# Kernel optimization log

Hardware: AMD Instinct MI355X
Metric: run time of the kernel (lower is better)

## Reference

```python
import jax, jax.numpy as jnp
import numpy as np

B, S, D = 2, 1024, 2048
H, G, DK, DV = 16, 4, 128, 128
E, K, F = 8, 2, 4096
EPS = 1e-6


def _rms_norm(x, w):
    return x * jax.lax.rsqrt(jnp.mean(x * x, axis=-1, keepdims=True) + EPS) * w


def _rope(x):
    # x: [B, S, h, d]; rotate-half RoPE with base 10000
    d = x.shape[-1]
    half = d // 2
    inv_freq = 1.0 / (10000.0 ** (jnp.arange(half, dtype=jnp.float32) / half))
    ang = jnp.arange(x.shape[1], dtype=jnp.float32)[:, None] * inv_freq[None, :]  # [S, half]
    cos = jnp.cos(ang)[None, :, None, :]
    sin = jnp.sin(ang)[None, :, None, :]
    x1, x2 = x[..., :half], x[..., half:]
    return jnp.concatenate([x1 * cos - x2 * sin, x1 * sin + x2 * cos], axis=-1)


def setup_inputs() -> dict:
    key = jax.random.key(0)
    ks = jax.random.split(key, 10)
    s = lambda *shape: 1.0 / np.sqrt(shape[-2] if len(shape) > 1 else shape[0])
    inp = {
        "x": jax.random.normal(ks[0], (B, S, D), jnp.float32),
        "ln1_w": jnp.ones((D,), jnp.float32),
        "Wq": jax.random.normal(ks[1], (D, H * DK), jnp.float32) * (D ** -0.5),
        "Wk": jax.random.normal(ks[2], (D, G * DK), jnp.float32) * (D ** -0.5),
        "Wv": jax.random.normal(ks[3], (D, G * DV), jnp.float32) * (D ** -0.5),
        "Wo": jax.random.normal(ks[4], (H * DV, D), jnp.float32) * ((H * DV) ** -0.5),
        "ln2_w": jnp.ones((D,), jnp.float32),
        "Wr": jax.random.normal(ks[5], (D, E), jnp.float32) * (D ** -0.5),
        "W1": jax.random.normal(ks[6], (E, D, F), jnp.float32) * (D ** -0.5),
        "W2": jax.random.normal(ks[7], (E, F, D), jnp.float32) * (F ** -0.5),
    }
    return inp


def reference(x, ln1_w, Wq, Wk, Wv, Wo, ln2_w, Wr, W1, W2):
    # --- GQA attention (pre-norm, residual) ---
    h = _rms_norm(x, ln1_w)
    q = (h @ Wq).reshape(B, S, H, DK)
    k = (h @ Wk).reshape(B, S, G, DK)
    v = (h @ Wv).reshape(B, S, G, DV)
    q = _rope(q)
    k = _rope(k)
    # expand KV groups to all heads: each group serves H // G query heads
    rep = H // G
    k = jnp.repeat(k, rep, axis=2)  # [B, S, H, DK]
    v = jnp.repeat(v, rep, axis=2)  # [B, S, H, DV]
    scores = jnp.einsum("bshd,bthd->bhst", q, k) * (DK ** -0.5)  # [B,H,S,S]
    causal = jnp.tril(jnp.ones((S, S), bool))
    scores = jnp.where(causal[None, None], scores, jnp.finfo(scores.dtype).min)
    probs = jax.nn.softmax(scores, axis=-1)
    attn = jnp.einsum("bhst,bthd->bshd", probs, v).reshape(B, S, H * DV)
    x = x + attn @ Wo

    # --- top-k MoE MLP (pre-norm, residual) ---
    h = _rms_norm(x, ln2_w)
    t = h.reshape(B * S, D)  # tokens
    logits = t @ Wr  # [T, E]
    top_vals, top_idx = jax.lax.top_k(logits, K)
    gates = jax.nn.softmax(top_vals, axis=-1)  # [T, K]
    # dense combine weights [T, E] (zero for non-selected experts)
    comb = jnp.zeros((B * S, E), t.dtype)
    comb = comb.at[jnp.arange(B * S)[:, None], top_idx].set(gates)
    # dense all-expert compute (reference form of the grouped GEMM)
    mid = jax.nn.silu(jnp.einsum("td,edf->tef", t, W1))  # [T, E, F]
    out_e = jnp.einsum("tef,efd->ted", mid, W2)          # [T, E, D]
    moe = jnp.einsum("te,ted->td", comb, out_e).reshape(B, S, D)
    return x + moe
```

## Files before the change

### kernel.cpp

```cpp
#include <hip/hip_runtime.h>

typedef unsigned short u16;
typedef __attribute__((ext_vector_type(8))) short bf16x8;
typedef __attribute__((ext_vector_type(4))) float f32x4;

__device__ __forceinline__ u16 f2bf(float f) {
  union { float f; unsigned u; } v; v.f = f;
  unsigned r = (v.u + 0x7fffu + ((v.u >> 16) & 1u)) >> 16;
  return (u16)r;
}
__device__ __forceinline__ float bf2f(u16 u) {
  union { unsigned u; float f; } v; v.u = ((unsigned)u) << 16;
  return v.f;
}
__device__ __forceinline__ void split2(float f, u16& hi, u16& lo) {
  hi = f2bf(f);
  lo = f2bf(f - bf2f(hi));
}

typedef const unsigned int __attribute__((address_space(1)))* gptr_t;
typedef unsigned int __attribute__((address_space(3)))* lptr_t;

__device__ __forceinline__ void gl16(const u16* g, u16* l) {
#if __has_builtin(__builtin_amdgcn_global_load_lds)
  __builtin_amdgcn_global_load_lds((gptr_t)g, (lptr_t)l, 16, 0, 0);
#else
  *reinterpret_cast<uint4*>(l) = *reinterpret_cast<const uint4*>(g);
#endif
}


__device__ __forceinline__ void mf_bf16(const u16* __restrict__ sA,
    const u16* __restrict__ sB, f32x4 (&acc)[4][4], int wm, int wn, int lr, int lk) {
  bf16x8 a[4], b[4];
#pragma unroll
  for (int i = 0; i < 4; i++) {
    a[i] = *reinterpret_cast<const bf16x8*>(&sA[(wm + i * 16 + lr) * 32 + lk]);
    b[i] = *reinterpret_cast<const bf16x8*>(&sB[(wn + i * 16 + lr) * 32 + lk]);
  }
#pragma unroll
  for (int i = 0; i < 4; i++)
#pragma unroll
    for (int j = 0; j < 4; j++)
      acc[i][j] = __builtin_amdgcn_mfma_f32_16x16x32_bf16(a[i], b[j], acc[i][j], 0, 0, 0);
}

__device__ __forceinline__ void mf_hilo(const u16* __restrict__ sAhp,
    const u16* __restrict__ sAlp, const u16* __restrict__ sBhp,
    const u16* __restrict__ sBlp, f32x4 (&acc)[4][4], int wm, int wn, int lr, int lk) {
  bf16x8 ah[4], al[4], bh[4], bl[4];
#pragma unroll
  for (int i = 0; i < 4; i++) {
    ah[i] = *reinterpret_cast<const bf16x8*>(&sAhp[(wm + i * 16 + lr) * 32 + lk]);
    al[i] = *reinterpret_cast<const bf16x8*>(&sAlp[(wm + i * 16 + lr) * 32 + lk]);
    bh[i] = *reinterpret_cast<const bf16x8*>(&sBhp[(wn + i * 16 + lr) * 32 + lk]);
    bl[i] = *reinterpret_cast<const bf16x8*>(&sBlp[(wn + i * 16 + lr) * 32 + lk]);
  }
#pragma unroll
  for (int i = 0; i < 4; i++)
#pragma unroll
    for (int j = 0; j < 4; j++) {
      f32x4 t = acc[i][j];
      t = __builtin_amdgcn_mfma_f32_16x16x32_bf16(al[i], bh[j], t, 0, 0, 0);
      t = __builtin_amdgcn_mfma_f32_16x16x32_bf16(ah[i], bl[j], t, 0, 0, 0);
      t = __builtin_amdgcn_mfma_f32_16x16x32_bf16(ah[i], bh[j], t, 0, 0, 0);
      acc[i][j] = t;
    }
}

#define HILO_PREAMBLE \
  __shared__ __align__(16) u16 sAh[2][4096], sAl[2][4096], sBh[2][4096], sBl[2][4096]; \
  int tid = threadIdx.x, lane = tid & 63; \
  int wm = ((tid >> 6) & 1) << 6, wn = (tid >> 7) << 6; \
  int lr = lane & 15, lk = (lane >> 4) << 3; \
  int er = (lane >> 4) << 2, ec = lane & 15; \
  int r = tid >> 2, c = (tid & 3) << 3; \
  int so = r * 32 + c, so2 = so + 2048; \
  f32x4 acc[4][4] = {};

#define STAGE_HILO(buf) \
  gl16(pAh + ko, &sAh[buf][so]); gl16(pAh2 + ko, &sAh[buf][so2]); \
  gl16(pAl + ko, &sAl[buf][so]); gl16(pAl2 + ko, &sAl[buf][so2]); \
  gl16(pBh + ko, &sBh[buf][so]); gl16(pBh2 + ko, &sBh[buf][so2]); \
  gl16(pBl + ko, &sBl[buf][so]); gl16(pBl2 + ko, &sBl[buf][so2]);

#define BF16_PREAMBLE \
  __shared__ __align__(16) u16 sA[2][4096], sB[2][4096]; \
  int tid = threadIdx.x, lane = tid & 63; \
  int wm = ((tid >> 6) & 1) << 6, wn = (tid >> 7) << 6; \
  int lr = lane & 15, lk = (lane >> 4) << 3; \
  int er = (lane >> 4) << 2, ec = lane & 15; \
  int r = tid >> 2, c = (tid & 3) << 3; \
  int so = r * 32 + c, so2 = so + 2048; \
  f32x4 acc[4][4] = {};

#define STAGE_AB(buf) \
  gl16(pA + ko, &sA[buf][so]); gl16(pA2 + ko, &sA[buf][so2]); \
  gl16(pB + ko, &sB[buf][so]); gl16(pB2 + ko, &sB[buf][so2]);

__global__ __launch_bounds__(256) void convt_bf16(const float* __restrict__ W,
    u16* __restrict__ T, int K, int N) {
  __shared__ float t[64][33];
  long eo = (long)blockIdx.z * K * N;
  int k0 = blockIdx.y << 6, n0 = blockIdx.x << 5;
  int tid = threadIdx.x;
  int r = tid >> 3, cc = (tid & 7) << 2;
  const float* src = W + eo + (long)(k0 + r) * N + n0 + cc;
  float4 a = *reinterpret_cast<const float4*>(src);
  float4 b = *reinterpret_cast<const float4*>(src + (long)32 * N);
  t[r][cc] = a.x; t[r][cc + 1] = a.y; t[r][cc + 2] = a.z; t[r][cc + 3] = a.w;
  t[r + 32][cc] = b.x; t[r + 32][cc + 1] = b.y; t[r + 32][cc + 2] = b.z; t[r + 32][cc + 3] = b.w;
  __syncthreads();
  int n = tid >> 3, kc = (tid & 7) << 3;
  __align__(16) u16 h[8];
#pragma unroll
  for (int i = 0; i < 8; i++) h[i] = f2bf(t[kc + i][n]);
  *reinterpret_cast<uint4*>(&T[eo + (long)(n0 + n) * K + k0 + kc]) =
      *reinterpret_cast<uint4*>(h);
}

__global__ __launch_bounds__(256) void convt_split(const float* __restrict__ W,
    u16* __restrict__ Thi, u16* __restrict__ Tlo, int K, int N) {
  __shared__ float t[64][33];
  int k0 = blockIdx.y << 6, n0 = blockIdx.x << 5;
  int tid = threadIdx.x;
  int r = tid >> 3, cc = (tid & 7) << 2;
  const float* src = W + (long)(k0 + r) * N + n0 + cc;
  float4 a = *reinterpret_cast<const float4*>(src);
  float4 b = *reinterpret_cast<const float4*>(src + (long)32 * N);
  t[r][cc] = a.x; t[r][cc + 1] = a.y; t[r][cc + 2] = a.z; t[r][cc + 3] = a.w;
  t[r + 32][cc] = b.x; t[r + 32][cc + 1] = b.y; t[r + 32][cc + 2] = b.z; t[r + 32][cc + 3] = b.w;
  __syncthreads();
  int n = tid >> 3, kc = (tid & 7) << 3;
  __align__(16) u16 h[8], l[8];
#pragma unroll
  for (int i = 0; i < 8; i++) split2(t[kc + i][n], h[i], l[i]);
  long o = (long)(n0 + n) * K + k0 + kc;
  *reinterpret_cast<uint4*>(&Thi[o]) = *reinterpret_cast<uint4*>(h);
  *reinterpret_cast<uint4*>(&Tlo[o]) = *reinterpret_cast<uint4*>(l);
}


__global__ __launch_bounds__(256) void rmsnorm_split(const float* __restrict__ x,
    const float* __restrict__ w, u16* __restrict__ ohi, u16* __restrict__ olo) {
  __shared__ float lbuf[4];
  int tid = threadIdx.x;
  long base = (long)blockIdx.x * 2048;
  float4 v0 = *reinterpret_cast<const float4*>(&x[base + tid * 8]);
  float4 v1 = *reinterpret_cast<const float4*>(&x[base + tid * 8 + 4]);
  float ss = v0.x * v0.x + v0.y * v0.y + v0.z * v0.z + v0.w * v0.w +
             v1.x * v1.x + v1.y * v1.y + v1.z * v1.z + v1.w * v1.w;
  for (int off = 32; off; off >>= 1) ss += __shfl_down(ss, off);
  if ((tid & 63) == 0) lbuf[tid >> 6] = ss;
  __syncthreads();
  float tot = lbuf[0] + lbuf[1] + lbuf[2] + lbuf[3];
  float scale = 1.0f / sqrtf(tot * (1.0f / 2048.0f) + 1e-6f);
  float4 w0 = *reinterpret_cast<const float4*>(&w[tid * 8]);
  float4 w1 = *reinterpret_cast<const float4*>(&w[tid * 8 + 4]);
  float f[8] = {v0.x * scale * w0.x, v0.y * scale * w0.y, v0.z * scale * w0.z,
                v0.w * scale * w0.w, v1.x * scale * w1.x, v1.y * scale * w1.y,
                v1.z * scale * w1.z, v1.w * scale * w1.w};
  __align__(16) u16 h[8], l[8];
#pragma unroll
  for (int i = 0; i < 8; i++) split2(f[i], h[i], l[i]);
  *reinterpret_cast<uint4*>(&ohi[base + tid * 8]) = *reinterpret_cast<uint4*>(h);
  *reinterpret_cast<uint4*>(&olo[base + tid * 8]) = *reinterpret_cast<uint4*>(l);
}

__global__ __launch_bounds__(256) void rmsnorm_bf16(const float* __restrict__ x,
    const float* __restrict__ w, u16* __restrict__ o) {
  __shared__ float lbuf[4];
  int tid = threadIdx.x;
  long base = (long)blockIdx.x * 2048;
  float4 v0 = *reinterpret_cast<const float4*>(&x[base + tid * 8]);
  float4 v1 = *reinterpret_cast<const float4*>(&x[base + tid * 8 + 4]);
  float ss = v0.x * v0.x + v0.y * v0.y + v0.z * v0.z + v0.w * v0.w +
             v1.x * v1.x + v1.y * v1.y + v1.z * v1.z + v1.w * v1.w;
  for (int off = 32; off; off >>= 1) ss += __shfl_down(ss, off);
  if ((tid & 63) == 0) lbuf[tid >> 6] = ss;
  __syncthreads();
  float tot = lbuf[0] + lbuf[1] + lbuf[2] + lbuf[3];
  float scale = 1.0f / sqrtf(tot * (1.0f / 2048.0f) + 1e-6f);
  float4 w0 = *reinterpret_cast<const float4*>(&w[tid * 8]);
  float4 w1 = *reinterpret_cast<const float4*>(&w[tid * 8 + 4]);
  ushort4 o0, o1;
  o0.x = f2bf(v0.x * scale * w0.x); o0.y = f2bf(v0.y * scale * w0.y);
  o0.z = f2bf(v0.z * scale * w0.z); o0.w = f2bf(v0.w * scale * w0.w);
  o1.x = f2bf(v1.x * scale * w1.x); o1.y = f2bf(v1.y * scale * w1.y);
  o1.z = f2bf(v1.z * scale * w1.z); o1.w = f2bf(v1.w * scale * w1.w);
  *reinterpret_cast<ushort4*>(&o[base + tid * 8]) = o0;
  *reinterpret_cast<ushort4*>(&o[base + tid * 8 + 4]) = o1;
}

__global__ __launch_bounds__(256) void rope_split(const float* __restrict__ x, int nh,
    u16* __restrict__ ohi, u16* __restrict__ olo) {
  int unit = blockIdx.x * 4 + (threadIdx.x >> 6);
  int lane = threadIdx.x & 63;
  int s = (unit / nh) & 1023;
  const float* p = x + (long)unit * 128;
  float x1 = p[lane], x2 = p[lane + 64];
  float ang = (float)s * exp2f((float)lane * (-13.287712379549449f / 64.0f));
  float sn, cs;
  sincosf(ang, &sn, &cs);
  long o = (long)unit * 128 + lane;
  u16 hh, ll;
  split2(x1 * cs - x2 * sn, hh, ll);
  ohi[o] = hh; olo[o] = ll;
  split2(x1 * sn + x2 * cs, hh, ll);
  ohi[o + 64] = hh; olo[o + 64] = ll;
}

__global__ __launch_bounds__(256) void transpose_split(const float* __restrict__ in,
    u16* __restrict__ ohi, u16* __restrict__ olo, int R, int C) {
  __shared__ float tile[32][33];
  long bo = (long)blockIdx.z * R * C;
  int r0 = blockIdx.y * 32, c0 = blockIdx.x * 32;
  int r = threadIdx.x >> 5, c = threadIdx.x & 31;
#pragma unroll
  for (int i = 0; i < 4; i++)
    tile[r + i * 8][c] = in[bo + (long)(r0 + r + i * 8) * C + c0 + c];
  __syncthreads();
#pragma unroll
  for (int i = 0; i < 4; i++) {
    u16 hh, ll;
    split2(tile[c][r + i * 8], hh, ll);
    long o = bo + (long)(c0 + r + i * 8) * R + r0 + c;
    ohi[o] = hh; olo[o] = ll;
  }
}

__global__ __launch_bounds__(256) void softmax_split(const float* __restrict__ sc,
    u16* __restrict__ phi, u16* __restrict__ plo) {
  __shared__ float lbuf[4];
  long row = blockIdx.x;
  int q = (int)(row & 1023);
  const float* p = sc + row * 1024;
  int tid = threadIdx.x;
  int valid = q + 1;
  int pend = (q & ~127) + 128;
  float v[4];
  float mx = -1e30f;
#pragma unroll
  for (int i = 0; i < 4; i++) {
    int t = tid + i * 256;
    float f = (t < valid) ? p[t] : -1e30f;
    v[i] = f;
    mx = fmaxf(mx, f);
  }
  for (int off = 32; off; off >>= 1) mx = fmaxf(mx, __shfl_down(mx, off));
  if ((tid & 63) == 0) lbuf[tid >> 6] = mx;
  __syncthreads();
  float m = fmaxf(fmaxf(lbuf[0], lbuf[1]), fmaxf(lbuf[2], lbuf[3]));
  __syncthreads();
  float sum = 0.0f;
#pragma unroll
  for (int i = 0; i < 4; i++) {
    int t = tid + i * 256;
    float e = (t < valid) ? expf(v[i] - m) : 0.0f;
    v[i] = e;
    sum += e;
  }
  for (int off = 32; off; off >>= 1) sum += __shfl_down(sum, off);
  if ((tid & 63) == 0) lbuf[tid >> 6] = sum;
  __syncthreads();
  float inv = 1.0f / (lbuf[0] + lbuf[1] + lbuf[2] + lbuf[3]);
#pragma unroll
  for (int i = 0; i < 4; i++) {
    int t = tid + i * 256;
    if (t < valid) {
      u16 hh, ll;
      split2(v[i] * inv, hh, ll);
      phi[row * 1024 + t] = hh; plo[row * 1024 + t] = ll;
    } else if (t < pend) {
      phi[row * 1024 + t] = 0; plo[row * 1024 + t] = 0;
    }
  }
}

__global__ __launch_bounds__(256) void router_kernel(const float* __restrict__ xo,
    const float* __restrict__ w, const float* __restrict__ Wr,
    int* __restrict__ tok_e, float* __restrict__ tok_g, int* __restrict__ counts) {
  __shared__ float lbuf[32];
  int tid = threadIdx.x;
  long base = (long)blockIdx.x * 2048;
  float4 v0 = *reinterpret_cast<const float4*>(&xo[base + tid * 8]);
  float4 v1 = *reinterpret_cast<const float4*>(&xo[base + tid * 8 + 4]);
  float ss = v0.x * v0.x + v0.y * v0.y + v0.z * v0.z + v0.w * v0.w +
             v1.x * v1.x + v1.y * v1.y + v1.z * v1.z + v1.w * v1.w;
  for (int off = 32; off; off >>= 1) ss += __shfl_down(ss, off);
  if ((tid & 63) == 0) lbuf[tid >> 6] = ss;
  __syncthreads();
  float tot = lbuf[0] + lbuf[1] + lbuf[2] + lbuf[3];
  float scale = 1.0f / sqrtf(tot * (1.0f / 2048.0f) + 1e-6f);
  __syncthreads();
  float4 w0 = *reinterpret_cast<const float4*>(&w[tid * 8]);
  float4 w1 = *reinterpret_cast<const float4*>(&w[tid * 8 + 4]);
  float h[8] = {v0.x * scale * w0.x, v0.y * scale * w0.y, v0.z * scale * w0.z,
                v0.w * scale * w0.w, v1.x * scale * w1.x, v1.y * scale * w1.y,
                v1.z * scale * w1.z, v1.w * scale * w1.w};
  float part[8] = {0, 0, 0, 0, 0, 0, 0, 0};
#pragma unroll
  for (int j = 0; j < 8; j++) {
    const float* wr = Wr + (long)(tid * 8 + j) * 8;
    float4 a = *reinterpret_cast<const float4*>(wr);
    float4 b = *reinterpret_cast<const float4*>(wr + 4);
    part[0] += h[j] * a.x; part[1] += h[j] * a.y;
    part[2] += h[j] * a.z; part[3] += h[j] * a.w;
    part[4] += h[j] * b.x; part[5] += h[j] * b.y;
    part[6] += h[j] * b.z; part[7] += h[j] * b.w;
  }
#pragma unroll
  for (int e = 0; e < 8; e++) {
    float s = part[e];
    for (int off = 32; off; off >>= 1) s += __shfl_down(s, off);
    if ((tid & 63) == 0) lbuf[(tid >> 6) * 8 + e] = s;
  }
  __syncthreads();
  if (tid == 0) {
    float lg[8];
#pragma unroll
    for (int e = 0; e < 8; e++)
      lg[e] = lbuf[e] + lbuf[8 + e] + lbuf[16 + e] + lbuf[24 + e];
    int e1 = 0;
    for (int e = 1; e < 8; e++) if (lg[e] > lg[e1]) e1 = e;
    int e2 = -1;
    for (int e = 0; e < 8; e++) if (e != e1 && (e2 < 0 || lg[e] > lg[e2])) e2 = e;
    float ex = __expf(lg[e2] - lg[e1]);
    float g1 = 1.0f / (1.0f + ex);
    tok_e[blockIdx.x * 2] = e1; tok_e[blockIdx.x * 2 + 1] = e2;
    tok_g[blockIdx.x * 2] = g1; tok_g[blockIdx.x * 2 + 1] = 1.0f - g1;
    atomicAdd(&counts[e1], 1);
    atomicAdd(&counts[e2], 1);
  }
}

__global__ void scan8(const int* __restrict__ counts, int* __restrict__ offsets,
                      int* __restrict__ cursor) {
  if (threadIdx.x == 0) {
    int off = 0;
    for (int e = 0; e < 8; e++) { offsets[e] = off; off += counts[e]; cursor[e] = 0; }
  }
}

__global__ __launch_bounds__(256) void fill_lists(const int* __restrict__ tok_e,
    const float* __restrict__ tok_g, const int* __restrict__ offsets,
    int* __restrict__ cursor, int* __restrict__ ltok, float* __restrict__ lgate) {
  int idx = blockIdx.x * 256 + threadIdx.x;
  int token = idx >> 1;
  int e = tok_e[idx];
  float g = tok_g[idx];
  int pos = atomicAdd(&cursor[e], 1);
  int j = offsets[e] + pos;
  ltok[j] = token;
  lgate[j] = g;
}


__global__ __launch_bounds__(256) void gemm_hilo(
    const u16* __restrict__ Ahi, const u16* __restrict__ Alo, long ldA,
    const u16* __restrict__ Bhi, const u16* __restrict__ Blo, long ldB,
    const float* __restrict__ resid, float* __restrict__ C, long ldC, int Ksize) {
  HILO_PREAMBLE
  int m0 = blockIdx.y << 7, n0 = blockIdx.x << 7;
  const u16* pAh = Ahi + (long)(m0 + r) * ldA + c;  const u16* pAh2 = pAh + 64 * ldA;
  const u16* pAl = Alo + (long)(m0 + r) * ldA + c;  const u16* pAl2 = pAl + 64 * ldA;
  const u16* pBh = Bhi + (long)(n0 + r) * ldB + c;  const u16* pBh2 = pBh + 64 * ldB;
  const u16* pBl = Blo + (long)(n0 + r) * ldB + c;  const u16* pBl2 = pBl + 64 * ldB;
  { int ko = 0; STAGE_HILO(0) }
  __syncthreads();
  int cur = 0;
  for (int k0 = 0; k0 < Ksize; k0 += 32) {
    if (k0 + 32 < Ksize) { int ko = k0 + 32; STAGE_HILO(cur ^ 1) }
    mf_hilo(sAh[cur], sAl[cur], sBh[cur], sBl[cur], acc, wm, wn, lr, lk);
    __syncthreads();
    cur ^= 1;
  }
#pragma unroll
  for (int i = 0; i < 4; i++)
#pragma unroll
    for (int j = 0; j < 4; j++)
#pragma unroll
      for (int rr = 0; rr < 4; rr++) {
        long idx = (long)(m0 + wm + i * 16 + er + rr) * ldC + n0 + wn + j * 16 + ec;
        float v = acc[i][j][rr];
        C[idx] = resid ? resid[idx] + v : v;
      }
}

__global__ __launch_bounds__(256) void gemm_qk(
    const u16* __restrict__ qhi, const u16* __restrict__ qlo,
    const u16* __restrict__ khi, const u16* __restrict__ klo,
    float* __restrict__ sc, int bh0) {
  HILO_PREAMBLE
  int idx = blockIdx.x, mi = 0;
  while ((mi + 1) * (mi + 2) / 2 <= idx) mi++;
  int ni = idx - mi * (mi + 1) / 2;
  int bh = bh0 + blockIdx.y, b = bh >> 4, hd = bh & 15, g = hd >> 2;
  int m0 = mi << 7, n0 = ni << 7;
  const u16* pAh = qhi + (long)b * 2097152 + hd * 128 + (long)(m0 + r) * 2048 + c;
  const u16* pAh2 = pAh + 64 * 2048;
  const u16* pAl = qlo + (long)b * 2097152 + hd * 128 + (long)(m0 + r) * 2048 + c;
  const u16* pAl2 = pAl + 64 * 2048;
  const u16* pBh = khi + (long)b * 524288 + g * 128 + (long)(n0 + r) * 512 + c;
  const u16* pBh2 = pBh + 64 * 512;
  const u16* pBl = klo + (long)b * 524288 + g * 128 + (long)(n0 + r) * 512 + c;
  const u16* pBl2 = pBl + 64 * 512;
  { int ko = 0; STAGE_HILO(0) }
  __syncthreads();
  int cur = 0;
  for (int k0 = 0; k0 < 128; k0 += 32) {
    if (k0 + 32 < 128) { int ko = k0 + 32; STAGE_HILO(cur ^ 1) }
    mf_hilo(sAh[cur], sAl[cur], sBh[cur], sBl[cur], acc, wm, wn, lr, lk);
    __syncthreads();
    cur ^= 1;
  }
  float* Cb = sc + ((long)blockIdx.y * 1024 + m0) * 1024 + n0;
  const float scalef = 0.08838834764831845f;
#pragma unroll
  for (int i = 0; i < 4; i++)
#pragma unroll
    for (int j = 0; j < 4; j++)
#pragma unroll
      for (int rr = 0; rr < 4; rr++)
        Cb[(long)(wm + i * 16 + er + rr) * 1024 + wn + j * 16 + ec] =
            acc[i][j][rr] * scalef;
}

__global__ __launch_bounds__(256) void gemm_pv(
    const u16* __restrict__ phi, const u16* __restrict__ plo,
    const u16* __restrict__ vthi, const u16* __restrict__ vtlo,
    u16* __restrict__ athi, u16* __restrict__ atlo, int bh0) {
  HILO_PREAMBLE
  int m0 = blockIdx.x << 7;
  int bh = bh0 + blockIdx.y, b = bh >> 4, hd = bh & 15, g = hd >> 2;
  const u16* pAh = phi + (long)blockIdx.y * 1048576 + (long)(m0 + r) * 1024 + c;
  const u16* pAh2 = pAh + 64 * 1024;
  const u16* pAl = plo + (long)blockIdx.y * 1048576 + (long)(m0 + r) * 1024 + c;
  const u16* pAl2 = pAl + 64 * 1024;
  const u16* pBh = vthi + (long)(b * 4 + g) * 131072 + (long)r * 1024 + c;
  const u16* pBh2 = pBh + 64 * 1024;
  const u16* pBl = vtlo + (long)(b * 4 + g) * 131072 + (long)r * 1024 + c;
  const u16* pBl2 = pBl + 64 * 1024;
  int Klim = m0 + 128;
  { int ko = 0; STAGE_HILO(0) }
  __syncthreads();
  int cur = 0;
  for (int k0 = 0; k0 < Klim; k0 += 32) {
    if (k0 + 32 < Klim) { int ko = k0 + 32; STAGE_HILO(cur ^ 1) }
    mf_hilo(sAh[cur], sAl[cur], sBh[cur], sBl[cur], acc, wm, wn, lr, lk);
    __syncthreads();
    cur ^= 1;
  }
  long Cb = ((long)(b * 1024 + m0) * 16 + hd) * 128;
#pragma unroll
  for (int i = 0; i < 4; i++)
#pragma unroll
    for (int j = 0; j < 4; j++)
#pragma unroll
      for (int rr = 0; rr < 4; rr++) {
        u16 hh, ll;
        split2(acc[i][j][rr], hh, ll);
        long o = Cb + (long)(wm + i * 16 + er + rr) * 2048 + wn + j * 16 + ec;
        athi[o] = hh; atlo[o] = ll;
      }
}


__global__ __launch_bounds__(256) void gemm_moe1(const u16* __restrict__ t2,
    const u16* __restrict__ W1T, const int* __restrict__ offsets,
    const int* __restrict__ counts, const int* __restrict__ ltok,
    u16* __restrict__ mid) {
  int e = blockIdx.z;
  int cnt = counts[e];
  int m0 = blockIdx.y << 7;
  if (m0 >= cnt) return;
  BF16_PREAMBLE
  int off = offsets[e];
  int n0 = blockIdx.x << 7;
  int valid = cnt - m0; if (valid > 128) valid = 128;
  int rr0 = (r < valid) ? r : 0;
  int rr1 = (r + 64 < valid) ? (r + 64) : 0;
  const u16* pA = t2 + (long)ltok[off + m0 + rr0] * 2048 + c;
  const u16* pA2 = t2 + (long)ltok[off + m0 + rr1] * 2048 + c;
  const u16* pB = W1T + (long)e * 8388608 + (long)(n0 + r) * 2048 + c;
  const u16* pB2 = pB + 64 * 2048;
  { int ko = 0; STAGE_AB(0) }
  __syncthreads();
  int cur = 0;
  for (int k0 = 0; k0 < 2048; k0 += 32) {
    if (k0 + 32 < 2048) { int ko = k0 + 32; STAGE_AB(cur ^ 1) }
    mf_bf16(sA[cur], sB[cur], acc, wm, wn, lr, lk);
    __syncthreads();
    cur ^= 1;
  }
#pragma unroll
  for (int i = 0; i < 4; i++)
#pragma unroll
    for (int j = 0; j < 4; j++)
#pragma unroll
      for (int rr = 0; rr < 4; rr++) {
        int rowl = wm + i * 16 + er + rr;
        if (rowl < valid) {
          float v = acc[i][j][rr];
          v = v / (1.0f + __expf(-v));
          mid[(long)(off + m0 + rowl) * 4096 + n0 + wn + j * 16 + ec] = f2bf(v);
        }
      }
}

__global__ __launch_bounds__(256) void gemm_moe2(const u16* __restrict__ mid,
    const u16* __restrict__ W2T, const int* __restrict__ offsets,
    const int* __restrict__ counts, const int* __restrict__ ltok,
    const float* __restrict__ lgate, float* __restrict__ out) {
  int e = blockIdx.z;
  int cnt = counts[e];
  int m0 = blockIdx.y << 7;
  if (m0 >= cnt) return;
  BF16_PREAMBLE
  int off = offsets[e];
  int n0 = blockIdx.x << 7;
  int valid = cnt - m0; if (valid > 128) valid = 128;
  int rw0 = off + m0 + ((r < valid) ? r : valid - 1);
  int rw1 = off + m0 + ((r + 64 < valid) ? r + 64 : valid - 1);
  const u16* pA = mid + (long)rw0 * 4096 + c;
  const u16* pA2 = mid + (long)rw1 * 4096 + c;
  const u16* pB = W2T + (long)e * 8388608 + (long)(n0 + r) * 4096 + c;
  const u16* pB2 = pB + 64 * 4096;
  { int ko = 0; STAGE_AB(0) }
  __syncthreads();
  int cur = 0;
  for (int k0 = 0; k0 < 4096; k0 += 32) {
    if (k0 + 32 < 4096) { int ko = k0 + 32; STAGE_AB(cur ^ 1) }
    mf_bf16(sA[cur], sB[cur], acc, wm, wn, lr, lk);
    __syncthreads();
    cur ^= 1;
  }
#pragma unroll
  for (int i = 0; i < 4; i++)
#pragma unroll
    for (int j = 0; j < 4; j++)
#pragma unroll
      for (int rr = 0; rr < 4; rr++) {
        int rowl = wm + i * 16 + er + rr;
        if (rowl < valid) {
          int t = ltok[off + m0 + rowl];
          float g = lgate[off + m0 + rowl];
          atomicAdd(&out[(long)t * 2048 + n0 + wn + j * 16 + ec], g * acc[i][j][rr]);
        }
      }
}

extern "C" void kernel_launch(void* const* d_in, const int* in_sizes, int n_in,
                              void* d_out, int out_size, void* d_ws, size_t ws_size,
                              hipStream_t stream) {
  (void)in_sizes; (void)n_in; (void)out_size; (void)ws_size;
  const float* x   = (const float*)d_in[0];
  const float* ln1 = (const float*)d_in[1];
  const float* Wq  = (const float*)d_in[2];
  const float* Wk  = (const float*)d_in[3];
  const float* Wv  = (const float*)d_in[4];
  const float* Wo  = (const float*)d_in[5];
  const float* ln2 = (const float*)d_in[6];
  const float* Wr  = (const float*)d_in[7];
  const float* W1  = (const float*)d_in[8];
  const float* W2  = (const float*)d_in[9];
  float* out = (float*)d_out;
  char* ws = (char*)d_ws;

  float* sc  = (float*)(ws);
  u16* phi   = (u16*)(ws + 33554432);
  u16* plo   = (u16*)(ws + 50331648);
  u16* hhi   = (u16*)(ws + 67108864);
  u16* hlo   = (u16*)(ws + 75497472);
  float* q   = (float*)(ws + 83886080);
  float* kk  = (float*)(ws + 100663296);
  float* vv  = (float*)(ws + 104857600);
  u16* qhi   = (u16*)(ws + 109051904);
  u16* qlo   = (u16*)(ws + 117440512);
  u16* khi   = (u16*)(ws + 125829120);
  u16* klo   = (u16*)(ws + 127926272);
  u16* vthi  = (u16*)(ws + 130023424);
  u16* vtlo  = (u16*)(ws + 132120576);
  u16* athi  = (u16*)(ws + 134217728);
  u16* atlo  = (u16*)(ws + 142606336);
  u16* wqh   = (u16*)(ws + 150994944);
  u16* wql   = (u16*)(ws + 159383552);
  u16* wkh   = (u16*)(ws + 167772160);
  u16* wkl   = (u16*)(ws + 169869312);
  u16* wvh   = (u16*)(ws + 171966464);
  u16* wvl   = (u16*)(ws + 174063616);
  u16* woh   = (u16*)(ws + 176160768);
  u16* wol   = (u16*)(ws + 184549376);
  u16* wbuf  = (u16*)(ws);
  u16* mid   = (u16*)(ws + 134217728);
  u16* t2    = (u16*)(ws + 167772160);
  char* misc = ws + 176160768;
  int*   tok_e   = (int*)misc;
  float* tok_g   = (float*)(misc + 16384);
  int*   ltok    = (int*)(misc + 32768);
  float* lgate   = (float*)(misc + 49152);
  int*   counts  = (int*)(misc + 65536);
  int*   offsets = (int*)(misc + 65600);
  int*   cursor  = (int*)(misc + 65664);

  convt_split<<<dim3(64, 32), 256, 0, stream>>>(Wq, wqh, wql, 2048, 2048);
  convt_split<<<dim3(16, 32), 256, 0, stream>>>(Wk, wkh, wkl, 2048, 512);
  convt_split<<<dim3(16, 32), 256, 0, stream>>>(Wv, wvh, wvl, 2048, 512);
  convt_split<<<dim3(64, 32), 256, 0, stream>>>(Wo, woh, wol, 2048, 2048);

  rmsnorm_split<<<2048, 256, 0, stream>>>(x, ln1, hhi, hlo);
  gemm_hilo<<<dim3(16, 16), 256, 0, stream>>>(hhi, hlo, 2048, wqh, wql, 2048,
                                              nullptr, q, 2048, 2048);
  gemm_hilo<<<dim3(4, 16), 256, 0, stream>>>(hhi, hlo, 2048, wkh, wkl, 2048,
                                             nullptr, kk, 512, 2048);
  gemm_hilo<<<dim3(4, 16), 256, 0, stream>>>(hhi, hlo, 2048, wvh, wvl, 2048,
                                             nullptr, vv, 512, 2048);
  rope_split<<<8192, 256, 0, stream>>>(q, 16, qhi, qlo);
  rope_split<<<2048, 256, 0, stream>>>(kk, 4, khi, klo);
  transpose_split<<<dim3(16, 32, 2), 256, 0, stream>>>(vv, vthi, vtlo, 1024, 512);
  for (int s = 0; s < 4; s++) {
    gemm_qk<<<dim3(36, 8), 256, 0, stream>>>(qhi, qlo, khi, klo, sc, s * 8);
    softmax_split<<<8192, 256, 0, stream>>>(sc, phi, plo);
    gemm_pv<<<dim3(8, 8), 256, 0, stream>>>(phi, plo, vthi, vtlo, athi, atlo, s * 8);
  }
  gemm_hilo<<<dim3(16, 16), 256, 0, stream>>>(athi, atlo, 2048, woh, wol, 2048,
                                              x, out, 2048, 2048);
  rmsnorm_bf16<<<2048, 256, 0, stream>>>(out, ln2, t2);
  hipMemsetAsync(counts, 0, 32, stream);
  router_kernel<<<2048, 256, 0, stream>>>(out, ln2, Wr, tok_e, tok_g, counts);
  scan8<<<1, 64, 0, stream>>>(counts, offsets, cursor);
  fill_lists<<<16, 256, 0, stream>>>(tok_e, tok_g, offsets, cursor, ltok, lgate);
  convt_bf16<<<dim3(128, 32, 8), 256, 0, stream>>>(W1, wbuf, 2048, 4096);
  gemm_moe1<<<dim3(32, 16, 8), 256, 0, stream>>>(t2, wbuf, offsets, counts, ltok, mid);
  convt_bf16<<<dim3(64, 64, 8), 256, 0, stream>>>(W2, wbuf, 4096, 2048);
  gemm_moe2<<<dim3(16, 16, 8), 256, 0, stream>>>(mid, wbuf, offsets, counts, ltok,
                                                 lgate, out);
}
```

Before: 1.566 ms.

## Split-K GEMMs, fuse QKV projection, and process all heads in one attention pass

Concatenates Wq/Wk/Wv into one weight and runs a single QKV GEMM with split-K over two partial buffers, which the RoPE and transpose kernels then sum. Attention now runs all 32 heads in one launch: QK writes hi/lo bf16 scores directly, softmax works in place on them, and PV is split by key tile over a triangular grid with atomic accumulation into fp32. Wo and MoE2 also use split-K with atomics, raising block count to fill more CUs. The cost is extra memsets, atomic traffic and additional partial-sum reads, and the fp32 accumulation order becomes nondeterministic.

```diff
diff --git a/kernel.cpp b/kernel.cpp
--- a/kernel.cpp
+++ b/kernel.cpp
@@ -28,7 +28,6 @@
   *reinterpret_cast<uint4*>(l) = *reinterpret_cast<const uint4*>(g);
 #endif
 }
-
 
 __device__ __forceinline__ void mf_bf16(const u16* __restrict__ sA,
     const u16* __restrict__ sB, f32x4 (&acc)[4][4], int wm, int wn, int lr, int lk) {
@@ -192,33 +191,39 @@
   *reinterpret_cast<ushort4*>(&o[base + tid * 8 + 4]) = o1;
 }
 
-__global__ __launch_bounds__(256) void rope_split(const float* __restrict__ x, int nh,
+__global__ __launch_bounds__(256) void rope2_split(const float* __restrict__ x0,
+    const float* __restrict__ x1, int hshift, int hmask, long ld, long colbase,
     u16* __restrict__ ohi, u16* __restrict__ olo) {
   int unit = blockIdx.x * 4 + (threadIdx.x >> 6);
   int lane = threadIdx.x & 63;
-  int s = (unit / nh) & 1023;
-  const float* p = x + (long)unit * 128;
-  float x1 = p[lane], x2 = p[lane + 64];
+  int s = (unit >> hshift) & 1023;
+  long src = (long)(unit >> hshift) * ld + colbase + ((long)(unit & hmask) << 7);
+  float a1 = x0[src + lane] + x1[src + lane];
+  float a2 = x0[src + lane + 64] + x1[src + lane + 64];
   float ang = (float)s * exp2f((float)lane * (-13.287712379549449f / 64.0f));
   float sn, cs;
   sincosf(ang, &sn, &cs);
   long o = (long)unit * 128 + lane;
   u16 hh, ll;
-  split2(x1 * cs - x2 * sn, hh, ll);
+  split2(a1 * cs - a2 * sn, hh, ll);
   ohi[o] = hh; olo[o] = ll;
-  split2(x1 * sn + x2 * cs, hh, ll);
+  split2(a1 * sn + a2 * cs, hh, ll);
   ohi[o + 64] = hh; olo[o + 64] = ll;
 }
 
-__global__ __launch_bounds__(256) void transpose_split(const float* __restrict__ in,
-    u16* __restrict__ ohi, u16* __restrict__ olo, int R, int C) {
+__global__ __launch_bounds__(256) void transpose2_split(const float* __restrict__ in0,
+    const float* __restrict__ in1, long ld, long bstride, u16* __restrict__ ohi,
+    u16* __restrict__ olo, int R, int C) {
   __shared__ float tile[32][33];
+  long bi = (long)blockIdx.z * bstride;
   long bo = (long)blockIdx.z * R * C;
   int r0 = blockIdx.y * 32, c0 = blockIdx.x * 32;
   int r = threadIdx.x >> 5, c = threadIdx.x & 31;
 #pragma unroll
-  for (int i = 0; i < 4; i++)
-    tile[r + i * 8][c] = in[bo + (long)(r0 + r + i * 8) * C + c0 + c];
+  for (int i = 0; i < 4; i++) {
+    long a = bi + (long)(r0 + r + i * 8) * ld + c0 + c;
+    tile[r + i * 8][c] = in0[a] + in1[a];
+  }
   __syncthreads();
 #pragma unroll
   for (int i = 0; i < 4; i++) {
@@ -229,23 +234,25 @@
   }
 }
 
-__global__ __launch_bounds__(256) void softmax_split(const float* __restrict__ sc,
-    u16* __restrict__ phi, u16* __restrict__ plo) {
+__global__ __launch_bounds__(256) void softmax_hilo(u16* __restrict__ ph,
+    u16* __restrict__ pl) {
   __shared__ float lbuf[4];
   long row = blockIdx.x;
   int q = (int)(row & 1023);
-  const float* p = sc + row * 1024;
   int tid = threadIdx.x;
   int valid = q + 1;
   int pend = (q & ~127) + 128;
-  float v[4];
+  int t0 = tid * 4;
+  long base = row * 1024 + t0;
+  ushort4 vh = *reinterpret_cast<ushort4*>(&ph[base]);
+  ushort4 vl = *reinterpret_cast<ushort4*>(&pl[base]);
+  float v[4] = {bf2f(vh.x) + bf2f(vl.x), bf2f(vh.y) + bf2f(vl.y),
+                bf2f(vh.z) + bf2f(vl.z), bf2f(vh.w) + bf2f(vl.w)};
   float mx = -1e30f;
 #pragma unroll
   for (int i = 0; i < 4; i++) {
-    int t = tid + i * 256;
-    float f = (t < valid) ? p[t] : -1e30f;
-    v[i] = f;
-    mx = fmaxf(mx, f);
+    if (t0 + i >= valid) v[i] = -1e30f;
+    mx = fmaxf(mx, v[i]);
   }
   for (int off = 32; off; off >>= 1) mx = fmaxf(mx, __shfl_down(mx, off));
   if ((tid & 63) == 0) lbuf[tid >> 6] = mx;
@@ -255,8 +262,7 @@
   float sum = 0.0f;
 #pragma unroll
   for (int i = 0; i < 4; i++) {
-    int t = tid + i * 256;
-    float e = (t < valid) ? expf(v[i] - m) : 0.0f;
+    float e = (t0 + i < valid) ? expf(v[i] - m) : 0.0f;
     v[i] = e;
     sum += e;
   }
@@ -264,17 +270,29 @@
   if ((tid & 63) == 0) lbuf[tid >> 6] = sum;
   __syncthreads();
   float inv = 1.0f / (lbuf[0] + lbuf[1] + lbuf[2] + lbuf[3]);
-#pragma unroll
-  for (int i = 0; i < 4; i++) {
-    int t = tid + i * 256;
-    if (t < valid) {
-      u16 hh, ll;
-      split2(v[i] * inv, hh, ll);
-      phi[row * 1024 + t] = hh; plo[row * 1024 + t] = ll;
-    } else if (t < pend) {
-      phi[row * 1024 + t] = 0; plo[row * 1024 + t] = 0;
-    }
-  }
+  if (t0 < pend) {
+    ushort4 oh, ol;
+    u16 hh, ll;
+    split2(v[0] * inv, hh, ll); oh.x = hh; ol.x = ll;
+    split2(v[1] * inv, hh, ll); oh.y = hh; ol.y = ll;
+    split2(v[2] * inv, hh, ll); oh.z = hh; ol.z = ll;
+    split2(v[3] * inv, hh, ll); oh.w = hh; ol.w = ll;
+    *reinterpret_cast<ushort4*>(&ph[base]) = oh;
+    *reinterpret_cast<ushort4*>(&pl[base]) = ol;
+  }
+}
+
+__global__ __launch_bounds__(256) void split_attn(const float* __restrict__ a,
+    u16* __restrict__ ohi, u16* __restrict__ olo) {
+  long i = ((long)blockIdx.x * 256 + threadIdx.x) * 8;
+  float4 v0 = *reinterpret_cast<const float4*>(&a[i]);
+  float4 v1 = *reinterpret_cast<const float4*>(&a[i + 4]);
+  float f[8] = {v0.x, v0.y, v0.z, v0.w, v1.x, v1.y, v1.z, v1.w};
+  __align__(16) u16 h[8], l[8];
+#pragma unroll
+  for (int j = 0; j < 8; j++) split2(f[j], h[j], l[j]);
+  *reinterpret_cast<uint4*>(&ohi[i]) = *reinterpret_cast<uint4*>(h);
+  *reinterpret_cast<uint4*>(&olo[i]) = *reinterpret_cast<uint4*>(l);
 }
 
 __global__ __launch_bounds__(256) void router_kernel(const float* __restrict__ xo,
@@ -356,46 +374,80 @@
 }
 
 
-__global__ __launch_bounds__(256) void gemm_hilo(
-    const u16* __restrict__ Ahi, const u16* __restrict__ Alo, long ldA,
-    const u16* __restrict__ Bhi, const u16* __restrict__ Blo, long ldB,
-    const float* __restrict__ resid, float* __restrict__ C, long ldC, int Ksize) {
+__global__ __launch_bounds__(256) void gemm_qkv(
+    const u16* __restrict__ Ahi, const u16* __restrict__ Alo,
+    const u16* __restrict__ Bhi, const u16* __restrict__ Blo,
+    float* __restrict__ C0, float* __restrict__ C1) {
   HILO_PREAMBLE
   int m0 = blockIdx.y << 7, n0 = blockIdx.x << 7;
-  const u16* pAh = Ahi + (long)(m0 + r) * ldA + c;  const u16* pAh2 = pAh + 64 * ldA;
-  const u16* pAl = Alo + (long)(m0 + r) * ldA + c;  const u16* pAl2 = pAl + 64 * ldA;
-  const u16* pBh = Bhi + (long)(n0 + r) * ldB + c;  const u16* pBh2 = pBh + 64 * ldB;
-  const u16* pBl = Blo + (long)(n0 + r) * ldB + c;  const u16* pBl2 = pBl + 64 * ldB;
+  long kb = (long)blockIdx.z << 10;
+  const u16* pAh = Ahi + (long)(m0 + r) * 2048 + kb + c;  const u16* pAh2 = pAh + 64 * 2048;
+  const u16* pAl = Alo + (long)(m0 + r) * 2048 + kb + c;  const u16* pAl2 = pAl + 64 * 2048;
+  const u16* pBh = Bhi + (long)(n0 + r) * 2048 + kb + c;  const u16* pBh2 = pBh + 64 * 2048;
+  const u16* pBl = Blo + (long)(n0 + r) * 2048 + kb + c;  const u16* pBl2 = pBl + 64 * 2048;
   { int ko = 0; STAGE_HILO(0) }
   __syncthreads();
   int cur = 0;
-  for (int k0 = 0; k0 < Ksize; k0 += 32) {
-    if (k0 + 32 < Ksize) { int ko = k0 + 32; STAGE_HILO(cur ^ 1) }
+  for (int k0 = 0; k0 < 1024; k0 += 32) {
+    if (k0 + 32 < 1024) { int ko = k0 + 32; STAGE_HILO(cur ^ 1) }
     mf_hilo(sAh[cur], sAl[cur], sBh[cur], sBl[cur], acc, wm, wn, lr, lk);
     __syncthreads();
     cur ^= 1;
   }
+  float* C = blockIdx.z ? C1 : C0;
 #pragma unroll
   for (int i = 0; i < 4; i++)
 #pragma unroll
     for (int j = 0; j < 4; j++)
 #pragma unroll
+      for (int rr = 0; rr < 4; rr++)
+        C[(long)(m0 + wm + i * 16 + er + rr) * 3072 + n0 + wn + j * 16 + ec] =
+            acc[i][j][rr];
+}
+
+__global__ __launch_bounds__(256) void gemm_wo(
+    const u16* __restrict__ Ahi, const u16* __restrict__ Alo,
+    const u16* __restrict__ Bhi, const u16* __restrict__ Blo,
+    const float* __restrict__ resid, float* __restrict__ C) {
+  HILO_PREAMBLE
+  int m0 = blockIdx.y << 7, n0 = blockIdx.x << 7;
+  long kb = (long)blockIdx.z << 10;
+  const u16* pAh = Ahi + (long)(m0 + r) * 2048 + kb + c;  const u16* pAh2 = pAh + 64 * 2048;
+  const u16* pAl = Alo + (long)(m0 + r) * 2048 + kb + c;  const u16* pAl2 = pAl + 64 * 2048;
+  const u16* pBh = Bhi + (long)(n0 + r) * 2048 + kb + c;  const u16* pBh2 = pBh + 64 * 2048;
+  const u16* pBl = Blo + (long)(n0 + r) * 2048 + kb + c;  const u16* pBl2 = pBl + 64 * 2048;
+  { int ko = 0; STAGE_HILO(0) }
+  __syncthreads();
+  int cur = 0;
+  for (int k0 = 0; k0 < 1024; k0 += 32) {
+    if (k0 + 32 < 1024) { int ko = k0 + 32; STAGE_HILO(cur ^ 1) }
+    mf_hilo(sAh[cur], sAl[cur], sBh[cur], sBl[cur], acc, wm, wn, lr, lk);
+    __syncthreads();
+    cur ^= 1;
+  }
+  int addres = (blockIdx.z == 0);
+#pragma unroll
+  for (int i = 0; i < 4; i++)
+#pragma unroll
+    for (int j = 0; j < 4; j++)
+#pragma unroll
       for (int rr = 0; rr < 4; rr++) {
-        long idx = (long)(m0 + wm + i * 16 + er + rr) * ldC + n0 + wn + j * 16 + ec;
+        long idx = (long)(m0 + wm + i * 16 + er + rr) * 2048 + n0 + wn + j * 16 + ec;
         float v = acc[i][j][rr];
-        C[idx] = resid ? resid[idx] + v : v;
+        if (addres) v += resid[idx];
+        atomicAdd(&C[idx], v);
       }
 }
 
 __global__ __launch_bounds__(256) void gemm_qk(
     const u16* __restrict__ qhi, const u16* __restrict__ qlo,
     const u16* __restrict__ khi, const u16* __restrict__ klo,
-    float* __restrict__ sc, int bh0) {
+    u16* __restrict__ schi, u16* __restrict__ sclo) {
   HILO_PREAMBLE
   int idx = blockIdx.x, mi = 0;
   while ((mi + 1) * (mi + 2) / 2 <= idx) mi++;
   int ni = idx - mi * (mi + 1) / 2;
-  int bh = bh0 + blockIdx.y, b = bh >> 4, hd = bh & 15, g = hd >> 2;
+  int bh = blockIdx.y, b = bh >> 4, hd = bh & 15, g = hd >> 2;
   int m0 = mi << 7, n0 = ni << 7;
   const u16* pAh = qhi + (long)b * 2097152 + hd * 128 + (long)(m0 + r) * 2048 + c;
   const u16* pAh2 = pAh + 64 * 2048;
@@ -414,39 +466,45 @@
     __syncthreads();
     cur ^= 1;
   }
-  float* Cb = sc + ((long)blockIdx.y * 1024 + m0) * 1024 + n0;
+  long Cb = (long)bh * 1048576 + (long)m0 * 1024 + n0;
   const float scalef = 0.08838834764831845f;
 #pragma unroll
   for (int i = 0; i < 4; i++)
 #pragma unroll
     for (int j = 0; j < 4; j++)
 #pragma unroll
-      for (int rr = 0; rr < 4; rr++)
-        Cb[(long)(wm + i * 16 + er + rr) * 1024 + wn + j * 16 + ec] =
-            acc[i][j][rr] * scalef;
-}
-
-__global__ __launch_bounds__(256) void gemm_pv(
+      for (int rr = 0; rr < 4; rr++) {
+        u16 hh, ll;
+        split2(acc[i][j][rr] * scalef, hh, ll);
+        long o = Cb + (long)(wm + i * 16 + er + rr) * 1024 + wn + j * 16 + ec;
+        schi[o] = hh; sclo[o] = ll;
+      }
+}
+
+__global__ __launch_bounds__(256) void gemm_pv_tri(
     const u16* __restrict__ phi, const u16* __restrict__ plo,
     const u16* __restrict__ vthi, const u16* __restrict__ vtlo,
-    u16* __restrict__ athi, u16* __restrict__ atlo, int bh0) {
+    float* __restrict__ attnf) {
   HILO_PREAMBLE
-  int m0 = blockIdx.x << 7;
-  int bh = bh0 + blockIdx.y, b = bh >> 4, hd = bh & 15, g = hd >> 2;
-  const u16* pAh = phi + (long)blockIdx.y * 1048576 + (long)(m0 + r) * 1024 + c;
+  int idx = blockIdx.x, mi = 0;
+  while ((mi + 1) * (mi + 2) / 2 <= idx) mi++;
+  int ki = idx - mi * (mi + 1) / 2;
+  int bh = blockIdx.y, b = bh >> 4, hd = bh & 15, g = hd >> 2;
+  int m0 = mi << 7;
+  long kb = (long)ki << 7;
+  const u16* pAh = phi + (long)bh * 1048576 + (long)(m0 + r) * 1024 + kb + c;
   const u16* pAh2 = pAh + 64 * 1024;
-  const u16* pAl = plo + (long)blockIdx.y * 1048576 + (long)(m0 + r) * 1024 + c;
+  const u16* pAl = plo + (long)bh * 1048576 + (long)(m0 + r) * 1024 + kb + c;
   const u16* pAl2 = pAl + 64 * 1024;
-  const u16* pBh = vthi + (long)(b * 4 + g) * 131072 + (long)r * 1024 + c;
+  const u16* pBh = vthi + (long)(b * 4 + g) * 131072 + (long)r * 1024 + kb + c;
   const u16* pBh2 = pBh + 64 * 1024;
-  const u16* pBl = vtlo + (long)(b * 4 + g) * 131072 + (long)r * 1024 + c;
+  const u16* pBl = vtlo + (long)(b * 4 + g) * 131072 + (long)r * 1024 + kb + c;
   const u16* pBl2 = pBl + 64 * 1024;
-  int Klim = m0 + 128;
   { int ko = 0; STAGE_HILO(0) }
   __syncthreads();
   int cur = 0;
-  for (int k0 = 0; k0 < Klim; k0 += 32) {
-    if (k0 + 32 < Klim) { int ko = k0 + 32; STAGE_HILO(cur ^ 1) }
+  for (int k0 = 0; k0 < 128; k0 += 32) {
+    if (k0 + 32 < 128) { int ko = k0 + 32; STAGE_HILO(cur ^ 1) }
     mf_hilo(sAh[cur], sAl[cur], sBh[cur], sBl[cur], acc, wm, wn, lr, lk);
     __syncthreads();
     cur ^= 1;
@@ -457,12 +515,9 @@
 #pragma unroll
     for (int j = 0; j < 4; j++)
 #pragma unroll
-      for (int rr = 0; rr < 4; rr++) {
-        u16 hh, ll;
-        split2(acc[i][j][rr], hh, ll);
-        long o = Cb + (long)(wm + i * 16 + er + rr) * 2048 + wn + j * 16 + ec;
-        athi[o] = hh; atlo[o] = ll;
-      }
+      for (int rr = 0; rr < 4; rr++)
+        atomicAdd(&attnf[Cb + (long)(wm + i * 16 + er + rr) * 2048 + wn + j * 16 + ec],
+                  acc[i][j][rr]);
 }
 
 
@@ -514,23 +569,25 @@
     const float* __restrict__ lgate, float* __restrict__ out) {
   int e = blockIdx.z;
   int cnt = counts[e];
-  int m0 = blockIdx.y << 7;
+  int mt = blockIdx.y >> 1, ks = blockIdx.y & 1;
+  int m0 = mt << 7;
   if (m0 >= cnt) return;
   BF16_PREAMBLE
   int off = offsets[e];
   int n0 = blockIdx.x << 7;
+  long kb = (long)ks << 11;
   int valid = cnt - m0; if (valid > 128) valid = 128;
   int rw0 = off + m0 + ((r < valid) ? r : valid - 1);
   int rw1 = off + m0 + ((r + 64 < valid) ? r + 64 : valid - 1);
-  const u16* pA = mid + (long)rw0 * 4096 + c;
-  const u16* pA2 = mid + (long)rw1 * 4096 + c;
-  const u16* pB = W2T + (long)e * 8388608 + (long)(n0 + r) * 4096 + c;
+  const u16* pA = mid + (long)rw0 * 4096 + kb + c;
+  const u16* pA2 = mid + (long)rw1 * 4096 + kb + c;
+  const u16* pB = W2T + (long)e * 8388608 + (long)(n0 + r) * 4096 + kb + c;
   const u16* pB2 = pB + 64 * 4096;
   { int ko = 0; STAGE_AB(0) }
   __syncthreads();
   int cur = 0;
-  for (int k0 = 0; k0 < 4096; k0 += 32) {
-    if (k0 + 32 < 4096) { int ko = k0 + 32; STAGE_AB(cur ^ 1) }
+  for (int k0 = 0; k0 < 2048; k0 += 32) {
+    if (k0 + 32 < 2048) { int ko = k0 + 32; STAGE_AB(cur ^ 1) }
     mf_bf16(sA[cur], sB[cur], acc, wm, wn, lr, lk);
     __syncthreads();
     cur ^= 1;
@@ -567,33 +624,28 @@
   float* out = (float*)d_out;
   char* ws = (char*)d_ws;
 
-  float* sc  = (float*)(ws);
-  u16* phi   = (u16*)(ws + 33554432);
-  u16* plo   = (u16*)(ws + 50331648);
-  u16* hhi   = (u16*)(ws + 67108864);
-  u16* hlo   = (u16*)(ws + 75497472);
-  float* q   = (float*)(ws + 83886080);
-  float* kk  = (float*)(ws + 100663296);
-  float* vv  = (float*)(ws + 104857600);
-  u16* qhi   = (u16*)(ws + 109051904);
-  u16* qlo   = (u16*)(ws + 117440512);
-  u16* khi   = (u16*)(ws + 125829120);
-  u16* klo   = (u16*)(ws + 127926272);
-  u16* vthi  = (u16*)(ws + 130023424);
-  u16* vtlo  = (u16*)(ws + 132120576);
-  u16* athi  = (u16*)(ws + 134217728);
-  u16* atlo  = (u16*)(ws + 142606336);
-  u16* wqh   = (u16*)(ws + 150994944);
-  u16* wql   = (u16*)(ws + 159383552);
-  u16* wkh   = (u16*)(ws + 167772160);
-  u16* wkl   = (u16*)(ws + 169869312);
-  u16* wvh   = (u16*)(ws + 171966464);
-  u16* wvl   = (u16*)(ws + 174063616);
-  u16* woh   = (u16*)(ws + 176160768);
-  u16* wol   = (u16*)(ws + 184549376);
-  u16* wbuf  = (u16*)(ws);
-  u16* mid   = (u16*)(ws + 134217728);
-  u16* t2    = (u16*)(ws + 167772160);
+  u16* hhi    = (u16*)(ws);
+  u16* hlo    = (u16*)(ws + 8388608);
+  float* qkv0 = (float*)(ws + 16777216);
+  float* qkv1 = (float*)(ws + 41943040);
+  u16* wqkvh  = (u16*)(ws + 67108864);
+  u16* wqkvl  = (u16*)(ws + 79691776);
+  u16* schi   = (u16*)(ws);
+  u16* sclo   = (u16*)(ws + 67108864);
+  u16* athi   = (u16*)(ws + 134217728);
+  u16* atlo   = (u16*)(ws + 142606336);
+  u16* qhi    = (u16*)(ws + 150994944);
+  u16* qlo    = (u16*)(ws + 159383552);
+  float* attnf = (float*)(ws + 150994944);
+  u16* khi    = (u16*)(ws + 167772160);
+  u16* klo    = (u16*)(ws + 169869312);
+  u16* vthi   = (u16*)(ws + 171966464);
+  u16* vtlo   = (u16*)(ws + 174063616);
+  u16* woh    = (u16*)(ws + 176160768);
+  u16* wol    = (u16*)(ws + 184549376);
+  u16* wbuf = (u16*)(ws);
+  u16* mid  = (u16*)(ws + 134217728);
+  u16* t2   = (u16*)(ws + 167772160);
   char* misc = ws + 176160768;
   int*   tok_e   = (int*)misc;
   float* tok_g   = (float*)(misc + 16384);
@@ -603,28 +655,27 @@
   int*   offsets = (int*)(misc + 65600);
   int*   cursor  = (int*)(misc + 65664);
 
-  convt_split<<<dim3(64, 32), 256, 0, stream>>>(Wq, wqh, wql, 2048, 2048);
-  convt_split<<<dim3(16, 32), 256, 0, stream>>>(Wk, wkh, wkl, 2048, 512);
-  convt_split<<<dim3(16, 32), 256, 0, stream>>>(Wv, wvh, wvl, 2048, 512);
+  convt_split<<<dim3(64, 32), 256, 0, stream>>>(Wq, wqkvh, wqkvl, 2048, 2048);
+  convt_split<<<dim3(16, 32), 256, 0, stream>>>(Wk, wqkvh + 2048 * 2048,
+                                                wqkvl + 2048 * 2048, 2048, 512);
+  convt_split<<<dim3(16, 32), 256, 0, stream>>>(Wv, wqkvh + 2560 * 2048,
+                                                wqkvl + 2560 * 2048, 2048, 512);
   convt_split<<<dim3(64, 32), 256, 0, stream>>>(Wo, woh, wol, 2048, 2048);
 
   rmsnorm_split<<<2048, 256, 0, stream>>>(x, ln1, hhi, hlo);
-  gemm_hilo<<<dim3(16, 16), 256, 0, stream>>>(hhi, hlo, 2048, wqh, wql, 2048,
-                                              nullptr, q, 2048, 2048);
-  gemm_hilo<<<dim3(4, 16), 256, 0, stream>>>(hhi, hlo, 2048, wkh, wkl, 2048,
-                                             nullptr, kk, 512, 2048);
-  gemm_hilo<<<dim3(4, 16), 256, 0, stream>>>(hhi, hlo, 2048, wvh, wvl, 2048,
-                                             nullptr, vv, 512, 2048);
-  rope_split<<<8192, 256, 0, stream>>>(q, 16, qhi, qlo);
-  rope_split<<<2048, 256, 0, stream>>>(kk, 4, khi, klo);
-  transpose_split<<<dim3(16, 32, 2), 256, 0, stream>>>(vv, vthi, vtlo, 1024, 512);
-  for (int s = 0; s < 4; s++) {
-    gemm_qk<<<dim3(36, 8), 256, 0, stream>>>(qhi, qlo, khi, klo, sc, s * 8);
-    softmax_split<<<8192, 256, 0, stream>>>(sc, phi, plo);
-    gemm_pv<<<dim3(8, 8), 256, 0, stream>>>(phi, plo, vthi, vtlo, athi, atlo, s * 8);
-  }
-  gemm_hilo<<<dim3(16, 16), 256, 0, stream>>>(athi, atlo, 2048, woh, wol, 2048,
-                                              x, out, 2048, 2048);
+  gemm_qkv<<<dim3(24, 16, 2), 256, 0, stream>>>(hhi, hlo, wqkvh, wqkvl, qkv0, qkv1);
+  rope2_split<<<8192, 256, 0, stream>>>(qkv0, qkv1, 4, 15, 3072, 0, qhi, qlo);
+  rope2_split<<<2048, 256, 0, stream>>>(qkv0, qkv1, 2, 3, 3072, 2048, khi, klo);
+  transpose2_split<<<dim3(16, 32, 2), 256, 0, stream>>>(
+      qkv0 + 2560, qkv1 + 2560, 3072, 3145728, vthi, vtlo, 1024, 512);
+  gemm_qk<<<dim3(36, 32), 256, 0, stream>>>(qhi, qlo, khi, klo, schi, sclo);
+  softmax_hilo<<<32768, 256, 0, stream>>>(schi, sclo);
+  hipMemsetAsync(attnf, 0, 16777216, stream);
+  gemm_pv_tri<<<dim3(36, 32), 256, 0, stream>>>(schi, sclo, vthi, vtlo, attnf);
+  split_attn<<<2048, 256, 0, stream>>>(attnf, athi, atlo);
+  hipMemsetAsync(out, 0, 16777216, stream);
+  gemm_wo<<<dim3(16, 16, 2), 256, 0, stream>>>(athi, atlo, woh, wol, x, out);
+
   rmsnorm_bf16<<<2048, 256, 0, stream>>>(out, ln2, t2);
   hipMemsetAsync(counts, 0, 32, stream);
   router_kernel<<<2048, 256, 0, stream>>>(out, ln2, Wr, tok_e, tok_g, counts);
@@ -633,6 +684,6 @@
   convt_bf16<<<dim3(128, 32, 8), 256, 0, stream>>>(W1, wbuf, 2048, 4096);
   gemm_moe1<<<dim3(32, 16, 8), 256, 0, stream>>>(t2, wbuf, offsets, counts, ltok, mid);
   convt_bf16<<<dim3(64, 64, 8), 256, 0, stream>>>(W2, wbuf, 4096, 2048);
-  gemm_moe2<<<dim3(16, 16, 8), 256, 0, stream>>>(mid, wbuf, offsets, counts, ltok,
+  gemm_moe2<<<dim3(16, 32, 8), 256, 0, stream>>>(mid, wbuf, offsets, counts, ltok,
                                                  lgate, out);
 }
```

New measurement: 1.333 ms. 14.9% less time.
